# Performance work log

Hardware: AMD Instinct MI355X
Metric: run time of the kernel (lower is better)

## Reference

```python
import jax, jax.numpy as jnp
import numpy as np

DIM = 2048
N_HEADS = 16
KV_HEADS = 2 * 2  # 4
HEAD_DIM = DIM // N_HEADS  # 128
B, T = 2, 2048


def apply_rope(x, cos, sin):
    # Faithful to the source: x is replaced by its rotated version, then
    # multiplied by (sin + cos). x: [B,H,T,D], cos/sin: [T,D] broadcast.
    x1 = x[..., ::2]
    x2 = x[..., 1::2]
    rot = jnp.stack((-x2, x1), axis=-1).reshape(x.shape)
    return rot * sin + rot * cos


def setup_inputs() -> dict:
    key = jax.random.key(0)
    ks = jax.random.split(key, 8)
    x = jax.random.normal(ks[0], (B, T, DIM), dtype=jnp.float32)
    cos = jax.random.uniform(ks[1], (T, HEAD_DIM), dtype=jnp.float32)
    sin = jax.random.uniform(ks[2], (T, HEAD_DIM), dtype=jnp.float32)
    mask = jnp.tril(jnp.ones((T, T), dtype=bool))  # causal
    s = 1.0 / np.sqrt(DIM)
    Wq = jax.random.normal(ks[3], (DIM, DIM), dtype=jnp.float32) * s
    Wk = jax.random.normal(ks[4], (KV_HEADS * HEAD_DIM, DIM), dtype=jnp.float32) * s
    Wv = jax.random.normal(ks[5], (KV_HEADS * HEAD_DIM, DIM), dtype=jnp.float32) * s
    Wout = jax.random.normal(ks[6], (DIM, DIM), dtype=jnp.float32) * s
    bout = jax.random.normal(ks[7], (DIM,), dtype=jnp.float32) * s
    return {"x": x, "cos": cos, "sin": sin, "mask": mask,
            "Wq": Wq, "Wk": Wk, "Wv": Wv, "Wout": Wout, "bout": bout}


def reference(x, cos, sin, mask, Wq, Wk, Wv, Wout, bout):
    Bb, Tt, C = x.shape
    # projections (torch Linear: x @ W.T)
    q = (x @ Wq.T).reshape(Bb, Tt, N_HEADS, HEAD_DIM).transpose(0, 2, 1, 3)
    k = (x @ Wk.T).reshape(Bb, Tt, KV_HEADS, HEAD_DIM).transpose(0, 2, 1, 3)
    v = (x @ Wv.T).reshape(Bb, Tt, KV_HEADS, HEAD_DIM).transpose(0, 2, 1, 3)
    q = apply_rope(q, cos, sin)
    k = apply_rope(k, cos, sin)
    repeat = N_HEADS // KV_HEADS
    k = jnp.repeat(k, repeat, axis=1)  # [B,H,T,D]
    v = jnp.repeat(v, repeat, axis=1)
    attn = jnp.einsum("bhtd,bhsd->bhts", q, k) / np.sqrt(HEAD_DIM)
    attn = jnp.where(mask, attn, jnp.float32(-1e9))
    probs = jax.nn.softmax(attn, axis=-1)
    out = jnp.einsum("bhts,bhsd->bhtd", probs, v)
    out = out.transpose(0, 2, 1, 3).reshape(Bb, Tt, C)
    return out @ Wout.T + bout
```

## Files before the change

kernel.cpp:

```cpp
#include <hip/hip_runtime.h>

#define DEVI __device__ __forceinline__

typedef unsigned short u16;
typedef unsigned int u32;
typedef float f32x4 __attribute__((ext_vector_type(4)));
typedef __bf16 bf16x8 __attribute__((ext_vector_type(8)));
typedef unsigned short u16x4 __attribute__((ext_vector_type(4)));
typedef unsigned short u16x8 __attribute__((ext_vector_type(8)));
typedef int i32x4 __attribute__((ext_vector_type(4)));
typedef unsigned int u32x2 __attribute__((ext_vector_type(2)));

constexpr int BATCH = 2;
constexpr int T     = 2048;
constexpr int DIM   = 2048;
constexpr int NH    = 16;
constexpr int KVH   = 4;
constexpr int HD    = 128;
constexpr int NQKV  = DIM + 2 * KVH * HD;
constexpr int ROWS  = BATCH * T;
constexpr float SCALE = 0.08838834764831845f;
constexpr float SC2   = 0.08838834764831845f * 1.4426950408889634f;

DEVI u16 f2b(float f) {
  u32 u = __float_as_uint(f);
  return (u16)((u + 0x7fffu + ((u >> 16) & 1u)) >> 16);
}
DEVI float b2f(u16 u) { return __uint_as_float(((u32)u) << 16); }

DEVI u32 cvtpk(float lo, float hi) {
  u32 r;
  asm("v_cvt_pk_bf16_f32 %0, %1, %2" : "=v"(r) : "v"(lo), "v"(hi));
  return r;
}

DEVI f32x4 mfma16(bf16x8 a, bf16x8 b, f32x4 c) {
  return __builtin_amdgcn_mfma_f32_16x16x32_bf16(a, b, c, 0, 0, 0);
}
DEVI void gload16(const void* g, void* l) {
  __builtin_amdgcn_global_load_lds((const __attribute__((address_space(1))) void*)g,
                                   (__attribute__((address_space(3))) void*)l, 16, 0, 0);
}

__global__ void cvt_bf16_kernel(const float* __restrict__ in, u16* __restrict__ out, int n4) {
  int i = blockIdx.x * 256 + threadIdx.x;
  if (i >= n4) return;
  float4 v = *((const float4*)in + i);
  u16x4 o = { f2b(v.x), f2b(v.y), f2b(v.z), f2b(v.w) };
  *((u16x4*)out + i) = o;
}

__global__ void cs_kernel(const float* __restrict__ c, const float* __restrict__ s,
                          float* __restrict__ cs, int n) {
  int i = blockIdx.x * 256 + threadIdx.x;
  if (i < n) cs[i] = c[i] + s[i];
}

template<bool BF16OUT, bool BIAS>
__global__ __launch_bounds__(256) void gemm_bt_kernel(
    const u16* __restrict__ A, const u16* __restrict__ W,
    void* __restrict__ Cout, const float* __restrict__ bias,
    int M, int N, int K)
{
  constexpr int BK = 64;
  __shared__ u16 sA[128 * BK];
  __shared__ u16 sB[128 * BK];
  const int nbx = N >> 7;
  const int bx = blockIdx.x % nbx;
  const int by = blockIdx.x / nbx;
  const int m0 = by << 7, n0 = bx << 7;
  const int tid = threadIdx.x;
  const int w = tid >> 6, lane = tid & 63;
  const int wr = w >> 1, wc = w & 1;
  const int lq = lane & 15, lg = lane >> 4;

  f32x4 acc[4][4] = {};

  int srow[4], scb[4];
#pragma unroll
  for (int c = 0; c < 4; ++c) {
    int off = (w * 4 + c) * 1024 + lane * 16;
    srow[c] = off >> 7;
    scb[c]  = (off & 127) ^ ((srow[c] & 7) << 4);
  }

  for (int kt = 0; kt < K; kt += BK) {
#pragma unroll
    for (int c = 0; c < 4; ++c) {
      u16* la = sA + (w * 4 + c) * 512;
      u16* lb = sB + (w * 4 + c) * 512;
      gload16(A + (size_t)(m0 + srow[c]) * K + kt + (scb[c] >> 1), la);
      gload16(W + (size_t)(n0 + srow[c]) * K + kt + (scb[c] >> 1), lb);
    }
    __syncthreads();
#pragma unroll
    for (int ks = 0; ks < 2; ++ks) {
      bf16x8 af[4], bfr[4];
#pragma unroll
      for (int i = 0; i < 4; ++i) {
        int ra = wr * 64 + i * 16 + lq;
        int ca = (ks * 64 + lg * 16) ^ ((ra & 7) << 4);
        af[i] = *(const bf16x8*)((const char*)sA + ra * 128 + ca);
        int rb = wc * 64 + i * 16 + lq;
        int cb = (ks * 64 + lg * 16) ^ ((rb & 7) << 4);
        bfr[i] = *(const bf16x8*)((const char*)sB + rb * 128 + cb);
      }
#pragma unroll
      for (int i = 0; i < 4; ++i)
#pragma unroll
        for (int j = 0; j < 4; ++j)
          acc[i][j] = mfma16(af[i], bfr[j], acc[i][j]);
    }
    __syncthreads();
  }

  const int crow = m0 + wr * 64 + lg * 4;
  const int ccol = n0 + wc * 64 + lq;
#pragma unroll
  for (int j = 0; j < 4; ++j) {
    int col = ccol + j * 16;
    float bv = BIAS ? bias[col] : 0.0f;
#pragma unroll
    for (int i = 0; i < 4; ++i)
#pragma unroll
      for (int r = 0; r < 4; ++r) {
        size_t idx = (size_t)(crow + i * 16 + r) * N + col;
        float v = acc[i][j][r] + bv;
        if (BF16OUT) ((u16*)Cout)[idx] = f2b(v);
        else         ((float*)Cout)[idx] = v;
      }
  }
}

template<int NHEADS, int COLBASE>
__global__ void rope_kernel(const u16* __restrict__ Y, const float* __restrict__ cs,
                            u16* __restrict__ out)
{
  int pid = blockIdx.x * 256 + threadIdx.x;
  constexpr int TOTAL = ROWS * NHEADS * (HD / 2);
  if (pid >= TOTAL) return;
  int i  = pid & 63;
  int hr = pid >> 6;
  int h  = hr & (NHEADS - 1);
  int r  = hr / NHEADS;
  int t  = r & (T - 1);
  int b  = r >> 11;
  u32 y = *(const u32*)(Y + (size_t)r * NQKV + COLBASE + h * HD + 2 * i);
  float y0 = b2f((u16)(y & 0xffffu));
  float y1 = b2f((u16)(y >> 16));
  const float* cp = cs + t * HD + 2 * i;
  u32 o = (u32)f2b(-y1 * cp[0]) | ((u32)f2b(y0 * cp[1]) << 16);
  *(u32*)(out + (((size_t)(b * NHEADS + h) * T + t) * HD + 2 * i)) = o;
}

__global__ void vt_kernel(const u16* __restrict__ Y, u16* __restrict__ vt)
{
  int pid = blockIdx.x * 256 + threadIdx.x;
  constexpr int TOTAL = BATCH * KVH * HD * (T / 8);
  if (pid >= TOTAL) return;
  int tc = pid & 255;
  int d  = (pid >> 8) & 127;
  int kh = (pid >> 15) & 3;
  int b  = pid >> 17;
  const u16* src = Y + (size_t)(b * T + tc * 8) * NQKV + (DIM + KVH * HD) + kh * HD + d;
  u16x8 v;
#pragma unroll
  for (int j = 0; j < 8; ++j) v[j] = src[(size_t)j * NQKV];
  *(u16x8*)(vt + ((size_t)((b * KVH + kh) * HD + d) * T + tc * 8)) = v;
}

__global__ __launch_bounds__(256, 2) void attn_kernel(
    const u16* __restrict__ Qr, const u16* __restrict__ Kr,
    const u16* __restrict__ Vt, u16* __restrict__ Aout)
{
  __shared__ u16 ldsK[2][64 * 128];
  __shared__ u16 ldsV[2][128 * 64];
  __shared__ u16 ldsP[4][32 * 40];

  const int tid = threadIdx.x;
  const int w = tid >> 6, lane = tid & 63;
  const int lq = lane & 15, lg = lane >> 4;

  const int raw = blockIdx.x;
  const int bh = raw >> 4;
  const int qcr = raw & 15;
  const int qc = (bh & 16) ? (15 - qcr) : qcr;
  const int b = bh >> 4, h = bh & 15, kh = h >> 2;
  const int qb = qc << 7;
  const int qw0 = qb + w * 32;
  const int nst = 2 * qc + 2;

  bf16x8 qf[2][4];
  {
    const u16* Qp = Qr + ((size_t)bh * T + qw0 + lq) * HD + lg * 8;
#pragma unroll
    for (int qg = 0; qg < 2; ++qg)
#pragma unroll
      for (int ds = 0; ds < 4; ++ds)
        qf[qg][ds] = *(const bf16x8*)(Qp + qg * 16 * HD + ds * 32);
  }

  const u16* Kg = Kr + (size_t)(b * KVH + kh) * T * HD;
  const u16* Vg = Vt + (size_t)(b * KVH + kh) * HD * T;

  int kgo[4], klb[4], vgo[4], vlb[4];
  {
    const int vr = lane >> 3, vc = lane & 7;
#pragma unroll
    for (int i = 0; i < 4; ++i) {
      int krow = w * 16 + i * 4 + lg;
      kgo[i] = krow * HD + (((lq * 16) ^ ((krow & 7) << 4)) >> 1);
      klb[i] = (w * 16 + i * 4) * 128;
      int vrow = w * 32 + i * 8 + vr;
      vgo[i] = vrow * T + (((vc * 16) ^ ((vr & 7) << 4)) >> 1);
      vlb[i] = (w * 32 + i * 8) * 64;
    }
  }

  f32x4 accO[2][8] = {};
  float m[2]    = { -1e30f, -1e30f };
  float lsum[2] = { 0.f, 0.f };

#pragma unroll
  for (int i = 0; i < 4; ++i) {
    gload16(Kg + kgo[i], &ldsK[0][klb[i]]);
    gload16(Vg + vgo[i], &ldsV[0][vlb[i]]);
  }
  __syncthreads();

  int cur = 0;
  for (int t = 0; t < nst; ++t) {
    if (t + 1 < nst) {
      const u16* Kt  = Kg + (size_t)(t + 1) * 64 * HD;
      const u16* Vts = Vg + (t + 1) * 64;
#pragma unroll
      for (int i = 0; i < 4; ++i) {
        gload16(Kt + kgo[i],  &ldsK[cur ^ 1][klb[i]]);
        gload16(Vts + vgo[i], &ldsV[cur ^ 1][vlb[i]]);
      }
    }
    const int s0 = t << 6;
    if (s0 <= qw0 + 31) {
      const u16* Kb = ldsK[cur];
      const u16* Vb = ldsV[cur];
      f32x4 aS[2][4] = {};
#pragma unroll
      for (int si = 0; si < 4; ++si) {
#pragma unroll
        for (int ds = 0; ds < 4; ++ds) {
          const u16* kp = Kb + (si * 16 + lq) * 128 +
                          (((ds * 64 + lg * 16) ^ ((lq & 7) << 4)) >> 1);
          bf16x8 kf = *(const bf16x8*)kp;
          aS[0][si] = mfma16(kf, qf[0][ds], aS[0][si]);
          aS[1][si] = mfma16(kf, qf[1][ds], aS[1][si]);
        }
      }
      float pp[2][16];
#pragma unroll
      for (int qg = 0; qg < 2; ++qg) {
        const int qidx = qw0 + qg * 16 + lq;
        float pm = -1e30f;
#pragma unroll
        for (int si = 0; si < 4; ++si)
#pragma unroll
          for (int r = 0; r < 4; ++r) {
            int s = s0 + si * 16 + lg * 4 + r;
            float v = (s <= qidx) ? aS[qg][si][r] * SC2 : -1e9f;
            pp[qg][si * 4 + r] = v;
            pm = fmaxf(pm, v);
          }
        pm = fmaxf(pm, __shfl_xor(pm, 16));
        pm = fmaxf(pm, __shfl_xor(pm, 32));
        if (!__all(pm <= m[qg] + 11.5f)) {
          float mn = fmaxf(m[qg], pm);
          float al = __builtin_amdgcn_exp2f(m[qg] - mn);
          m[qg] = mn;
          lsum[qg] *= al;
#pragma unroll
          for (int db = 0; db < 8; ++db) accO[qg][db] *= al;
        }
        float ps = 0.f;
#pragma unroll
        for (int i2 = 0; i2 < 16; ++i2) {
          float e = __builtin_amdgcn_exp2f(pp[qg][i2] - m[qg]);
          pp[qg][i2] = e;
          ps += e;
        }
        ps += __shfl_xor(ps, 16);
        ps += __shfl_xor(ps, 32);
        lsum[qg] += ps;
      }
#pragma unroll
      for (int ks = 0; ks < 2; ++ks) {
#pragma unroll
        for (int qg = 0; qg < 2; ++qg) {
          u16* pw = &ldsP[w][(qg * 16 + lq) * 40];
          u32x2 wa = { cvtpk(pp[qg][8 * ks + 0], pp[qg][8 * ks + 1]),
                       cvtpk(pp[qg][8 * ks + 2], pp[qg][8 * ks + 3]) };
          u32x2 wb = { cvtpk(pp[qg][8 * ks + 4], pp[qg][8 * ks + 5]),
                       cvtpk(pp[qg][8 * ks + 6], pp[qg][8 * ks + 7]) };
          *(u32x2*)(pw + lg * 4)      = wa;
          *(u32x2*)(pw + 16 + lg * 4) = wb;
        }
        asm volatile("" ::: "memory");
        bf16x8 pf0 = *(const bf16x8*)(&ldsP[w][lq * 40] + lg * 8);
        bf16x8 pf1 = *(const bf16x8*)(&ldsP[w][(16 + lq) * 40] + lg * 8);
        asm volatile("" ::: "memory");
#pragma unroll
        for (int db = 0; db < 8; ++db) {
          const u16* vp = Vb + (db * 16 + lq) * 64 +
                          (((ks * 64 + lg * 16) ^ ((lq & 7) << 4)) >> 1);
          bf16x8 vf = *(const bf16x8*)vp;
          accO[0][db] = mfma16(vf, pf0, accO[0][db]);
          accO[1][db] = mfma16(vf, pf1, accO[1][db]);
        }
      }
    }
    __syncthreads();
    cur ^= 1;
  }

  u16* Ab = Aout + ((size_t)b * T + qw0) * DIM + h * HD;
#pragma unroll
  for (int qg = 0; qg < 2; ++qg) {
    float inv = 1.0f / lsum[qg];
#pragma unroll
    for (int db = 0; db < 8; ++db) {
      u32x2 st = { cvtpk(accO[qg][db][0] * inv, accO[qg][db][1] * inv),
                   cvtpk(accO[qg][db][2] * inv, accO[qg][db][3] * inv) };
      *(u32x2*)(Ab + (size_t)(qg * 16 + lq) * DIM + db * 16 + lg * 4) = st;
    }
  }
}

extern "C" void kernel_launch(void* const* d_in, const int* in_sizes, int n_in,
                              void* d_out, int out_size, void* d_ws, size_t ws_size,
                              hipStream_t stream) {
  const float* x    = (const float*)d_in[0];
  const float* cosp = (const float*)d_in[1];
  const float* sinp = (const float*)d_in[2];
  const float* Wq   = (const float*)d_in[4];
  const float* Wk   = (const float*)d_in[5];
  const float* Wv   = (const float*)d_in[6];
  const float* Wo   = (const float*)d_in[7];
  const float* bo   = (const float*)d_in[8];

  char* ws = (char*)d_ws;
  u16*   xb   = (u16*)(ws + 0);
  u16*   wqkv = (u16*)(ws + 16777216);
  u16*   wout = (u16*)(ws + 29360128);
  float* cs   = (float*)(ws + 37748736);
  u16*   yqkv = (u16*)(ws + 38797312);
  u16*   kr   = (u16*)(ws + 63963136);
  u16*   vt   = (u16*)(ws + 68157440);
  u16* qr   = xb;
  u16* aout = yqkv;

  cvt_bf16_kernel<<<ROWS * DIM / 4 / 256, 256, 0, stream>>>(x, xb, ROWS * DIM / 4);
  cvt_bf16_kernel<<<DIM * DIM / 4 / 256, 256, 0, stream>>>(Wq, wqkv, DIM * DIM / 4);
  cvt_bf16_kernel<<<512 * DIM / 4 / 256, 256, 0, stream>>>(Wk, wqkv + DIM * DIM, 512 * DIM / 4);
  cvt_bf16_kernel<<<512 * DIM / 4 / 256, 256, 0, stream>>>(Wv, wqkv + (size_t)(DIM + 512) * DIM, 512 * DIM / 4);
  cvt_bf16_kernel<<<DIM * DIM / 4 / 256, 256, 0, stream>>>(Wo, wout, DIM * DIM / 4);
  cs_kernel<<<T * HD / 256, 256, 0, stream>>>(cosp, sinp, cs, T * HD);

  gemm_bt_kernel<true, false><<<(ROWS / 128) * (NQKV / 128), 256, 0, stream>>>(
      xb, wqkv, yqkv, nullptr, ROWS, NQKV, DIM);

  rope_kernel<NH, 0><<<ROWS * NH * 64 / 256, 256, 0, stream>>>(yqkv, cs, qr);
  rope_kernel<KVH, DIM><<<ROWS * KVH * 64 / 256, 256, 0, stream>>>(yqkv, cs, kr);
  vt_kernel<<<BATCH * KVH * HD * (T / 8) / 256, 256, 0, stream>>>(yqkv, vt);

  attn_kernel<<<BATCH * NH * (T / 128), 256, 0, stream>>>(qr, kr, vt, aout);

  gemm_bt_kernel<false, true><<<(ROWS / 128) * (DIM / 128), 256, 0, stream>>>(
      aout, wout, d_out, bo, ROWS, DIM, DIM);
}
```

Measured before the change: 233.6 us.

## Pair mirrored query chunks per attention block, fold scale into RoPE, tile V transpose

Each attention block now handles two 64-row query chunks, one early and its mirror late, so every block does about the same causal work. Non-diagonal tiles skip masking, and MFMA sections are wrapped in s_setprio. The softmax scale is folded into Q during RoPE, and the V transpose goes through an LDS tile for coalesced reads and writes. This evens out load across blocks and trims per-element ALU work. The cost is more branch specialisation and a slightly different Q rounding to bf16 after scaling.

```diff
diff --git a/kernel.cpp b/kernel.cpp
--- a/kernel.cpp
+++ b/kernel.cpp
@@ -1,4 +1,5 @@
 #include <hip/hip_runtime.h>
+#include <type_traits>
 
 #define DEVI __device__ __forceinline__
 
@@ -134,7 +135,7 @@
 
 template<int NHEADS, int COLBASE>
 __global__ void rope_kernel(const u16* __restrict__ Y, const float* __restrict__ cs,
-                            u16* __restrict__ out)
+                            u16* __restrict__ out, float scale)
 {
   int pid = blockIdx.x * 256 + threadIdx.x;
   constexpr int TOTAL = ROWS * NHEADS * (HD / 2);
@@ -149,24 +150,34 @@
   float y0 = b2f((u16)(y & 0xffffu));
   float y1 = b2f((u16)(y >> 16));
   const float* cp = cs + t * HD + 2 * i;
-  u32 o = (u32)f2b(-y1 * cp[0]) | ((u32)f2b(y0 * cp[1]) << 16);
+  u32 o = (u32)f2b(-y1 * cp[0] * scale) | ((u32)f2b(y0 * cp[1] * scale) << 16);
   *(u32*)(out + (((size_t)(b * NHEADS + h) * T + t) * HD + 2 * i)) = o;
 }
 
-__global__ void vt_kernel(const u16* __restrict__ Y, u16* __restrict__ vt)
+__global__ __launch_bounds__(256) void vt_kernel(const u16* __restrict__ Y, u16* __restrict__ vt)
 {
-  int pid = blockIdx.x * 256 + threadIdx.x;
-  constexpr int TOTAL = BATCH * KVH * HD * (T / 8);
-  if (pid >= TOTAL) return;
-  int tc = pid & 255;
-  int d  = (pid >> 8) & 127;
-  int kh = (pid >> 15) & 3;
-  int b  = pid >> 17;
-  const u16* src = Y + (size_t)(b * T + tc * 8) * NQKV + (DIM + KVH * HD) + kh * HD + d;
-  u16x8 v;
-#pragma unroll
-  for (int j = 0; j < 8; ++j) v[j] = src[(size_t)j * NQKV];
-  *(u16x8*)(vt + ((size_t)((b * KVH + kh) * HD + d) * T + tc * 8)) = v;
+  __shared__ u16 tile[64][136];
+  const int tid = threadIdx.x;
+  const int tc = blockIdx.x & 31;
+  const int kh = (blockIdx.x >> 5) & 3;
+  const int b  = blockIdx.x >> 7;
+  const u16* src = Y + (size_t)(b * T + tc * 64) * NQKV + (DIM + KVH * HD) + kh * HD;
+#pragma unroll
+  for (int pass = 0; pass < 4; ++pass) {
+    int r = pass * 16 + (tid >> 4);
+    int c = (tid & 15) * 8;
+    *(u16x8*)&tile[r][c] = *(const u16x8*)(src + (size_t)r * NQKV + c);
+  }
+  __syncthreads();
+  const int d = tid >> 1, th = tid & 1;
+  u16* dst = vt + ((size_t)((b * KVH + kh) * HD + d) * T) + tc * 64 + th * 32;
+#pragma unroll
+  for (int j = 0; j < 4; ++j) {
+    u16x8 v;
+#pragma unroll
+    for (int e = 0; e < 8; ++e) v[e] = tile[th * 32 + j * 8 + e][d];
+    *(u16x8*)(dst + j * 8) = v;
+  }
 }
 
 __global__ __launch_bounds__(256, 2) void attn_kernel(
@@ -181,23 +192,23 @@
   const int w = tid >> 6, lane = tid & 63;
   const int lq = lane & 15, lg = lane >> 4;
 
-  const int raw = blockIdx.x;
-  const int bh = raw >> 4;
-  const int qcr = raw & 15;
-  const int qc = (bh & 16) ? (15 - qcr) : qcr;
+  const int bh = blockIdx.x >> 4;
+  const int p  = blockIdx.x & 15;
   const int b = bh >> 4, h = bh & 15, kh = h >> 2;
-  const int qb = qc << 7;
-  const int qw0 = qb + w * 32;
-  const int nst = 2 * qc + 2;
+  const int qcA = p, qcB = 31 - p;
+  const int rowA = qcA * 64 + w * 16;
+  const int rowB = qcB * 64 + w * 16;
+  const int nst = qcB + 1;
 
   bf16x8 qf[2][4];
   {
-    const u16* Qp = Qr + ((size_t)bh * T + qw0 + lq) * HD + lg * 8;
-#pragma unroll
-    for (int qg = 0; qg < 2; ++qg)
-#pragma unroll
-      for (int ds = 0; ds < 4; ++ds)
-        qf[qg][ds] = *(const bf16x8*)(Qp + qg * 16 * HD + ds * 32);
+    const u16* QpA = Qr + ((size_t)bh * T + rowA + lq) * HD + lg * 8;
+    const u16* QpB = Qr + ((size_t)bh * T + rowB + lq) * HD + lg * 8;
+#pragma unroll
+    for (int ds = 0; ds < 4; ++ds) {
+      qf[0][ds] = *(const bf16x8*)(QpA + ds * 32);
+      qf[1][ds] = *(const bf16x8*)(QpB + ds * 32);
+    }
   }
 
   const u16* Kg = Kr + (size_t)(b * KVH + kh) * T * HD;
@@ -240,95 +251,127 @@
       }
     }
     const int s0 = t << 6;
-    if (s0 <= qw0 + 31) {
-      const u16* Kb = ldsK[cur];
-      const u16* Vb = ldsV[cur];
+    const u16* Kb = ldsK[cur];
+    const u16* Vb = ldsV[cur];
+
+    auto softmax_qg = [&](f32x4 (&s4)[4], int qidx, bool diag, float& mm, float& ls,
+                          f32x4 (&aO)[8], float (&pp)[16]) {
+      float pm = -1e30f;
+      if (diag) {
+#pragma unroll
+        for (int si = 0; si < 4; ++si)
+#pragma unroll
+          for (int r = 0; r < 4; ++r) {
+            int s = s0 + si * 16 + lg * 4 + r;
+            float v = (s <= qidx) ? s4[si][r] : -1e9f;
+            pp[si * 4 + r] = v; pm = fmaxf(pm, v);
+          }
+      } else {
+#pragma unroll
+        for (int si = 0; si < 4; ++si)
+#pragma unroll
+          for (int r = 0; r < 4; ++r) {
+            float v = s4[si][r];
+            pp[si * 4 + r] = v; pm = fmaxf(pm, v);
+          }
+      }
+      pm = fmaxf(pm, __shfl_xor(pm, 16));
+      pm = fmaxf(pm, __shfl_xor(pm, 32));
+      if (!__all(pm <= mm + 11.5f)) {
+        float mn = fmaxf(mm, pm);
+        float al = __builtin_amdgcn_exp2f(mm - mn);
+        mm = mn; ls *= al;
+#pragma unroll
+        for (int db = 0; db < 8; ++db) aO[db] *= al;
+      }
+      float ps = 0.f;
+#pragma unroll
+      for (int i2 = 0; i2 < 16; ++i2) {
+        float e = __builtin_amdgcn_exp2f(pp[i2] - mm);
+        pp[i2] = e; ps += e;
+      }
+      ps += __shfl_xor(ps, 16);
+      ps += __shfl_xor(ps, 32);
+      ls += ps;
+    };
+
+    auto tile_body = [&](auto hasA_c) {
+      constexpr bool HASA = decltype(hasA_c)::value;
       f32x4 aS[2][4] = {};
-#pragma unroll
-      for (int si = 0; si < 4; ++si) {
+      __builtin_amdgcn_s_setprio(1);
+#pragma unroll
+      for (int si = 0; si < 4; ++si)
 #pragma unroll
         for (int ds = 0; ds < 4; ++ds) {
           const u16* kp = Kb + (si * 16 + lq) * 128 +
                           (((ds * 64 + lg * 16) ^ ((lq & 7) << 4)) >> 1);
           bf16x8 kf = *(const bf16x8*)kp;
-          aS[0][si] = mfma16(kf, qf[0][ds], aS[0][si]);
+          if constexpr (HASA) aS[0][si] = mfma16(kf, qf[0][ds], aS[0][si]);
           aS[1][si] = mfma16(kf, qf[1][ds], aS[1][si]);
         }
-      }
+      __builtin_amdgcn_s_setprio(0);
+
       float pp[2][16];
-#pragma unroll
-      for (int qg = 0; qg < 2; ++qg) {
-        const int qidx = qw0 + qg * 16 + lq;
-        float pm = -1e30f;
-#pragma unroll
-        for (int si = 0; si < 4; ++si)
-#pragma unroll
-          for (int r = 0; r < 4; ++r) {
-            int s = s0 + si * 16 + lg * 4 + r;
-            float v = (s <= qidx) ? aS[qg][si][r] * SC2 : -1e9f;
-            pp[qg][si * 4 + r] = v;
-            pm = fmaxf(pm, v);
-          }
-        pm = fmaxf(pm, __shfl_xor(pm, 16));
-        pm = fmaxf(pm, __shfl_xor(pm, 32));
-        if (!__all(pm <= m[qg] + 11.5f)) {
-          float mn = fmaxf(m[qg], pm);
-          float al = __builtin_amdgcn_exp2f(m[qg] - mn);
-          m[qg] = mn;
-          lsum[qg] *= al;
-#pragma unroll
-          for (int db = 0; db < 8; ++db) accO[qg][db] *= al;
+      if constexpr (HASA)
+        softmax_qg(aS[0], rowA + lq, t == qcA, m[0], lsum[0], accO[0], pp[0]);
+      softmax_qg(aS[1], rowB + lq, t == qcB, m[1], lsum[1], accO[1], pp[1]);
+
+#pragma unroll
+      for (int ks = 0; ks < 2; ++ks) {
+        if constexpr (HASA) {
+          u16* pw = &ldsP[w][lq * 40];
+          u32x2 wa = { cvtpk(pp[0][8 * ks + 0], pp[0][8 * ks + 1]),
+                       cvtpk(pp[0][8 * ks + 2], pp[0][8 * ks + 3]) };
+          u32x2 wb = { cvtpk(pp[0][8 * ks + 4], pp[0][8 * ks + 5]),
+                       cvtpk(pp[0][8 * ks + 6], pp[0][8 * ks + 7]) };
+          *(u32x2*)(pw + lg * 4)      = wa;
+          *(u32x2*)(pw + 16 + lg * 4) = wb;
         }
-        float ps = 0.f;
-#pragma unroll
-        for (int i2 = 0; i2 < 16; ++i2) {
-          float e = __builtin_amdgcn_exp2f(pp[qg][i2] - m[qg]);
-          pp[qg][i2] = e;
-          ps += e;
-        }
-        ps += __shfl_xor(ps, 16);
-        ps += __shfl_xor(ps, 32);
-        lsum[qg] += ps;
-      }
-#pragma unroll
-      for (int ks = 0; ks < 2; ++ks) {
-#pragma unroll
-        for (int qg = 0; qg < 2; ++qg) {
-          u16* pw = &ldsP[w][(qg * 16 + lq) * 40];
-          u32x2 wa = { cvtpk(pp[qg][8 * ks + 0], pp[qg][8 * ks + 1]),
-                       cvtpk(pp[qg][8 * ks + 2], pp[qg][8 * ks + 3]) };
-          u32x2 wb = { cvtpk(pp[qg][8 * ks + 4], pp[qg][8 * ks + 5]),
-                       cvtpk(pp[qg][8 * ks + 6], pp[qg][8 * ks + 7]) };
+        {
+          u16* pw = &ldsP[w][(16 + lq) * 40];
+          u32x2 wa = { cvtpk(pp[1][8 * ks + 0], pp[1][8 * ks + 1]),
+                       cvtpk(pp[1][8 * ks + 2], pp[1][8 * ks + 3]) };
+          u32x2 wb = { cvtpk(pp[1][8 * ks + 4], pp[1][8 * ks + 5]),
+                       cvtpk(pp[1][8 * ks + 6], pp[1][8 * ks + 7]) };
           *(u32x2*)(pw + lg * 4)      = wa;
           *(u32x2*)(pw + 16 + lg * 4) = wb;
         }
         asm volatile("" ::: "memory");
-        bf16x8 pf0 = *(const bf16x8*)(&ldsP[w][lq * 40] + lg * 8);
-        bf16x8 pf1 = *(const bf16x8*)(&ldsP[w][(16 + lq) * 40] + lg * 8);
+        bf16x8 pf0, pf1;
+        if constexpr (HASA) pf0 = *(const bf16x8*)(&ldsP[w][lq * 40] + lg * 8);
+        pf1 = *(const bf16x8*)(&ldsP[w][(16 + lq) * 40] + lg * 8);
         asm volatile("" ::: "memory");
+        __builtin_amdgcn_s_setprio(1);
 #pragma unroll
         for (int db = 0; db < 8; ++db) {
           const u16* vp = Vb + (db * 16 + lq) * 64 +
                           (((ks * 64 + lg * 16) ^ ((lq & 7) << 4)) >> 1);
           bf16x8 vf = *(const bf16x8*)vp;
-          accO[0][db] = mfma16(vf, pf0, accO[0][db]);
+          if constexpr (HASA) accO[0][db] = mfma16(vf, pf0, accO[0][db]);
           accO[1][db] = mfma16(vf, pf1, accO[1][db]);
         }
-      }
-    }
+        __builtin_amdgcn_s_setprio(0);
+      }
+    };
+
+    if (t <= qcA) tile_body(std::integral_constant<bool, true>{});
+    else          tile_body(std::integral_constant<bool, false>{});
+
     __syncthreads();
     cur ^= 1;
   }
 
-  u16* Ab = Aout + ((size_t)b * T + qw0) * DIM + h * HD;
 #pragma unroll
   for (int qg = 0; qg < 2; ++qg) {
-    float inv = 1.0f / lsum[qg];
+    const int rowX = qg ? rowB : rowA;
+    float inv = 1.0f / (qg ? lsum[1] : lsum[0]);
+    u16* Ab = Aout + ((size_t)b * T + rowX + lq) * DIM + h * HD;
 #pragma unroll
     for (int db = 0; db < 8; ++db) {
-      u32x2 st = { cvtpk(accO[qg][db][0] * inv, accO[qg][db][1] * inv),
-                   cvtpk(accO[qg][db][2] * inv, accO[qg][db][3] * inv) };
-      *(u32x2*)(Ab + (size_t)(qg * 16 + lq) * DIM + db * 16 + lg * 4) = st;
+      f32x4 a = qg ? accO[1][db] : accO[0][db];
+      u32x2 st = { cvtpk(a[0] * inv, a[1] * inv),
+                   cvtpk(a[2] * inv, a[3] * inv) };
+      *(u32x2*)(Ab + db * 16 + lg * 4) = st;
     }
   }
 }
@@ -366,11 +409,11 @@
   gemm_bt_kernel<true, false><<<(ROWS / 128) * (NQKV / 128), 256, 0, stream>>>(
       xb, wqkv, yqkv, nullptr, ROWS, NQKV, DIM);
 
-  rope_kernel<NH, 0><<<ROWS * NH * 64 / 256, 256, 0, stream>>>(yqkv, cs, qr);
-  rope_kernel<KVH, DIM><<<ROWS * KVH * 64 / 256, 256, 0, stream>>>(yqkv, cs, kr);
-  vt_kernel<<<BATCH * KVH * HD * (T / 8) / 256, 256, 0, stream>>>(yqkv, vt);
-
-  attn_kernel<<<BATCH * NH * (T / 128), 256, 0, stream>>>(qr, kr, vt, aout);
+  rope_kernel<NH, 0><<<ROWS * NH * 64 / 256, 256, 0, stream>>>(yqkv, cs, qr, SC2);
+  rope_kernel<KVH, DIM><<<ROWS * KVH * 64 / 256, 256, 0, stream>>>(yqkv, cs, kr, 1.0f);
+  vt_kernel<<<BATCH * KVH * (T / 64), 256, 0, stream>>>(yqkv, vt);
+
+  attn_kernel<<<BATCH * NH * 16, 256, 0, stream>>>(qr, kr, vt, aout);
 
   gemm_bt_kernel<false, true><<<(ROWS / 128) * (DIM / 128), 256, 0, stream>>>(
       aout, wout, d_out, bo, ROWS, DIM, DIM);
```

After: 223.1 us. -4.5%, faster.
